# Kernel optimization log

Measured on AMD Instinct MI355X. Metric: run time of the kernel, lower is better.

Reference implementation:

```python
import jax, jax.numpy as jnp
import numpy as np

N_NODES = 150000
N_EDGES = 300000
N_LG_EDGES = 600000
N_TREE = 60000
HIDDEN = 256
DEPTH = 4
ATOM_FDIM = 35
BOND_FDIM = 5
NUM_GRAPHS = 2048


def setup_inputs() -> dict:
    key = jax.random.key(0)
    ks = jax.random.split(key, 14)
    return {
        "node_x": jax.random.normal(ks[0], (N_NODES, ATOM_FDIM), dtype=jnp.float32),
        "bond_x": jax.random.normal(ks[1], (N_EDGES, BOND_FDIM), dtype=jnp.float32),
        "tree_mess": jax.random.normal(ks[2], (N_TREE, HIDDEN), dtype=jnp.float32),
        "W_i": jax.random.normal(ks[3], (ATOM_FDIM + BOND_FDIM, HIDDEN), dtype=jnp.float32) * 0.05,
        "W_h": jax.random.normal(ks[4], (HIDDEN, HIDDEN), dtype=jnp.float32) * 0.05,
        "W_o": jax.random.normal(ks[5], (ATOM_FDIM + HIDDEN, HIDDEN), dtype=jnp.float32) * 0.05,
        "b_o": jax.random.normal(ks[6], (HIDDEN,), dtype=jnp.float32) * 0.05,
        "edge_src": jax.random.randint(ks[7], (N_EDGES,), 0, N_NODES, dtype=jnp.int64 if jax.config.jax_enable_x64 else jnp.int32).astype(jnp.int32),
        "edge_dst": jax.random.randint(ks[8], (N_EDGES,), 0, N_NODES).astype(jnp.int32),
        "lg_src": jax.random.randint(ks[9], (N_LG_EDGES,), 0, N_EDGES).astype(jnp.int32),
        "lg_dst": jax.random.randint(ks[10], (N_LG_EDGES,), 0, N_EDGES).astype(jnp.int32),
        "tgt_nodes": jax.random.randint(ks[11], (N_TREE,), 0, N_NODES).astype(jnp.int32),
        "graph_ids": jnp.sort(jax.random.randint(ks[12], (N_NODES,), 0, NUM_GRAPHS)).astype(jnp.int32),
        "num_graphs": NUM_GRAPHS,
    }


def reference(node_x, bond_x, tree_mess, W_i, W_h, W_o, b_o,
              edge_src, edge_dst, lg_src, lg_dst, tgt_nodes, graph_ids, num_graphs):
    n_nodes = node_x.shape[0]
    n_edges = bond_x.shape[0]

    # msg_input = W_i([src_atom_x ; bond_x])  (no bias)
    features = jnp.concatenate([node_x[edge_src], bond_x], axis=1)  # [E, 40]
    msg_input = features @ W_i                                       # [E, H]
    msg = jax.nn.relu(msg_input)

    # tree-message alpha: scatter_add tree messages onto target atoms (non-PAPER branch)
    node_alpha = jnp.zeros((n_nodes, msg.shape[1]), msg.dtype).at[tgt_nodes].add(tree_mess)
    edge_alpha = node_alpha[edge_src]  # apply_edges: alpha = src['alpha']

    # loopy BP on the line graph: accum = sum of incoming line-graph messages
    def body(msg, _):
        accum = jax.ops.segment_sum(msg[lg_src], lg_dst, num_segments=n_edges)
        msg = jax.nn.relu(msg_input + (accum + edge_alpha) @ W_h)
        return msg, None

    msg, _ = jax.lax.scan(body, msg, None, length=DEPTH - 1)

    # gather: m[v] = sum of msg over incoming edges; h = relu(W_o([x ; m + alpha]) + b)
    m = jax.ops.segment_sum(msg, edge_dst, num_segments=n_nodes)
    h = jax.nn.relu(jnp.concatenate([node_x, m + node_alpha], axis=1) @ W_o + b_o)

    # mean_nodes per graph
    counts = jax.ops.segment_sum(jnp.ones((n_nodes,), h.dtype), graph_ids, num_segments=num_graphs)
    g_sum = jax.ops.segment_sum(h, graph_ids, num_segments=num_graphs)
    g_repr = g_sum / jnp.maximum(counts, 1.0)[:, None]
    return g_repr
```

## Files before the change

### kernel.cpp

```cpp
#include <hip/hip_runtime.h>
#include <stdint.h>

#define HID 256
#define CAP 16

typedef __attribute__((ext_vector_type(8))) short bf16x8;
typedef __attribute__((ext_vector_type(4))) float f32x4;
typedef __attribute__((ext_vector_type(2))) float f32x2;

__device__ __forceinline__ float bf2f(unsigned short u) {
    union { unsigned int i; float f; } v; v.i = ((unsigned int)u) << 16; return v.f;
}
__device__ __forceinline__ unsigned short f2bf(float f) {
    union { float f; unsigned int i; } v; v.f = f;
    unsigned int r = (v.i + 0x7fffu + ((v.i >> 16) & 1u)) >> 16;
    return (unsigned short)r;
}
__device__ __forceinline__ float fp82f_sw(unsigned char b) {
    unsigned int s = (unsigned int)(b & 0x80) << 24;
    int e = (b >> 3) & 0xF;
    int m = b & 7;
    float v;
    if (e) v = __uint_as_float(((unsigned int)(e + 120) << 23) | ((unsigned int)m << 20));
    else   v = (float)m * 0.001953125f;
    return __uint_as_float(__float_as_uint(v) | s);
}
__device__ __forceinline__ unsigned char f2fp8_sw(float x) {
    unsigned int bits = __float_as_uint(x);
    unsigned char s = (unsigned char)((bits >> 24) & 0x80);
    float ax = fabsf(x);
    if (!(ax >= 0.001953125f)) {
        int n = (int)rintf(ax * 512.f);
        return s | (unsigned char)n;
    }
    if (ax >= 448.f) return s | 0x7E;
    int ex; float mant = frexpf(ax, &ex);
    int e = ex + 6;
    if (e >= 1) {
        int q = (int)rintf(mant * 16.f);
        if (q == 16) { q = 8; ++e; }
        if (e > 15 || (e == 15 && q > 14)) return s | 0x7E;
        return s | (unsigned char)((e << 3) | (q - 8));
    } else {
        int n = (int)rintf(ax * 512.f);
        if (n >= 8) return s | 0x08;
        return s | (unsigned char)n;
    }
}
__device__ __forceinline__ unsigned char f2fp8(float x) {
#if __has_builtin(__builtin_amdgcn_cvt_pk_fp8_f32)
    return (unsigned char)(__builtin_amdgcn_cvt_pk_fp8_f32(x, x, 0, false) & 0xff);
#else
    return f2fp8_sw(x);
#endif
}
__device__ __forceinline__ f32x4 fp8x4_to_f32(unsigned int u) {
#if __has_builtin(__builtin_amdgcn_cvt_pk_f32_fp8)
    f32x2 a = __builtin_amdgcn_cvt_pk_f32_fp8(u, false);
    f32x2 b = __builtin_amdgcn_cvt_pk_f32_fp8(u, true);
    f32x4 r; r[0] = a.x; r[1] = a.y; r[2] = b.x; r[3] = b.y;
    return r;
#else
    f32x4 r;
    #pragma unroll
    for (int q = 0; q < 4; ++q) r[q] = fp82f_sw((u >> (8 * q)) & 0xff);
    return r;
#endif
}
__device__ __forceinline__ bf16x8 fp8x8_to_bf16x8(uint2 raw) {
#if __has_builtin(__builtin_amdgcn_cvt_pk_f32_fp8)
    f32x2 p0 = __builtin_amdgcn_cvt_pk_f32_fp8(raw.x, false);
    f32x2 p1 = __builtin_amdgcn_cvt_pk_f32_fp8(raw.x, true);
    f32x2 p2 = __builtin_amdgcn_cvt_pk_f32_fp8(raw.y, false);
    f32x2 p3 = __builtin_amdgcn_cvt_pk_f32_fp8(raw.y, true);
    union { unsigned int u[4]; bf16x8 v; } cv;
    cv.u[0] = (__float_as_uint(p0.x) >> 16) | (__float_as_uint(p0.y) & 0xffff0000u);
    cv.u[1] = (__float_as_uint(p1.x) >> 16) | (__float_as_uint(p1.y) & 0xffff0000u);
    cv.u[2] = (__float_as_uint(p2.x) >> 16) | (__float_as_uint(p2.y) & 0xffff0000u);
    cv.u[3] = (__float_as_uint(p3.x) >> 16) | (__float_as_uint(p3.y) & 0xffff0000u);
    return cv.v;
#else
    union { unsigned short u[8]; bf16x8 v; } cv;
    #pragma unroll
    for (int q = 0; q < 4; ++q) cv.u[q]     = f2bf(fp82f_sw((raw.x >> (8 * q)) & 0xff));
    #pragma unroll
    for (int q = 0; q < 4; ++q) cv.u[4 + q] = f2bf(fp82f_sw((raw.y >> (8 * q)) & 0xff));
    return cv.v;
#endif
}

__device__ __forceinline__ void llds16(const void* g, void* l) {
    __builtin_amdgcn_global_load_lds(
        (const __attribute__((address_space(1))) void*)g,
        (__attribute__((address_space(3))) void*)l, 16, 0, 0);
}


__global__ void k_zero_f(float* __restrict__ p, size_t n) {
    size_t i = (size_t)blockIdx.x * 256 + threadIdx.x;
    if (i < n) p[i] = 0.f;
}
__global__ void k_diag(float* __restrict__ out, float v) {
    if (blockIdx.x == 0 && threadIdx.x == 0) out[0] = v;
}

__global__ void k_init(int* __restrict__ cnt_lg, int E,
                       int* __restrict__ cnt_nd, int* __restrict__ cnt_t, int N,
                       int* __restrict__ gcnt, int* __restrict__ gstart, int G) {
    int i = blockIdx.x * 256 + threadIdx.x;
    if (i < E) cnt_lg[i] = 0;
    if (i < N) { cnt_nd[i] = 0; cnt_t[i] = 0; }
    if (i < G) { gcnt[i] = 0; gstart[i] = N; }
}

__global__ void k_alpha(const float* __restrict__ tm, const int* __restrict__ cnt,
                        const int* __restrict__ bkt, unsigned char* __restrict__ alpha, int N) {
    int wave = threadIdx.x >> 6, lane = threadIdx.x & 63;
    int v = blockIdx.x * 4 + wave;
    if (v >= N) return;
    int d = cnt[v]; if (d > CAP) d = CAP;
    f32x4 s = {0.f, 0.f, 0.f, 0.f};
    const int* bb = bkt + (size_t)v * CAP;
    for (int t = 0; t < d; ++t) {
        int r = bb[t];
        f32x4 x = *(const f32x4*)(tm + (size_t)r * HID + lane * 4);
        #pragma unroll
        for (int k = 0; k < 4; ++k) s[k] += x[k];
    }
    union { unsigned char b[4]; unsigned int u; } ov;
    #pragma unroll
    for (int k = 0; k < 4; ++k) ov.b[k] = f2fp8(s[k]);
    *(unsigned int*)(alpha + (size_t)v * HID + lane * 4) = ov.u;
}

__global__ void k_wt_i(const float* __restrict__ W, unsigned short* __restrict__ Wt) {
    int i = blockIdx.x * 256 + threadIdx.x;
    int n = i >> 6, k = i & 63;
    Wt[i] = f2bf((k < 40) ? W[k * HID + n] : 0.f);
}
__global__ void k_wt_hi(const float* __restrict__ Wh, const float* __restrict__ Wi,
                        unsigned short* __restrict__ Wt) {
    int i = blockIdx.x * 256 + threadIdx.x;
    int n = i / 320, k = i % 320;
    float v;
    if (k < 256) v = Wh[(size_t)k * HID + n];
    else if (k < 296) v = Wi[(size_t)(k - 256) * HID + n];
    else v = 0.f;
    Wt[i] = f2bf(v);
}
__global__ void k_wt_o(const float* __restrict__ W, unsigned short* __restrict__ Wt) {
    int i = blockIdx.x * 256 + threadIdx.x;
    int n = i / 320, k = i % 320;
    float v;
    if (k < 256) v = W[(size_t)(35 + k) * HID + n];
    else if (k < 291) v = W[(size_t)(k - 256) * HID + n];
    else v = 0.f;
    Wt[i] = f2bf(v);
}

__global__ void k_a1(const float* __restrict__ nx, const float* __restrict__ bx,
                     const int* __restrict__ esrc, unsigned char* __restrict__ A1, int E) {
    int i = blockIdx.x * 256 + threadIdx.x;
    if (i >= E * 64) return;
    int e = i >> 6, k = i & 63;
    float v = 0.f;
    if (k < 35) v = nx[(size_t)esrc[e] * 35 + k];
    else if (k < 40) v = bx[(size_t)e * 5 + (k - 35)];
    A1[i] = f2fp8(v);
}

__global__ void k_x1(const float* __restrict__ nx, unsigned char* __restrict__ X1, int N) {
    int i = blockIdx.x * 256 + threadIdx.x;
    if (i >= N * 64) return;
    int v = i >> 6, k = i & 63;
    X1[i] = f2fp8((k < 35) ? nx[(size_t)v * 35 + k] : 0.f);
}

__global__ void k_fill(const int* __restrict__ dst, const int* __restrict__ val,
                       int* __restrict__ cnt, int* __restrict__ bkt, int n, int useval) {
    int i = blockIdx.x * 256 + threadIdx.x;
    if (i >= n) return;
    int d = dst[i];
    int p = atomicAdd(&cnt[d], 1);
    if (p < CAP) bkt[(size_t)d * CAP + p] = useval ? val[i] : i;
}

__global__ void k_gfill(const int* __restrict__ gid, int* __restrict__ gstart,
                        int* __restrict__ gcnt, int N) {
    int i = blockIdx.x * 256 + threadIdx.x;
    if (i >= N) return;
    int g = gid[i];
    atomicAdd(&gcnt[g], 1);
    atomicMin(&gstart[g], i);
}

template<int K1, int KTOT, int EPI, bool PF8, bool QF8, bool OUTF8>
__global__ __launch_bounds__(256, 2)
void gemm4(const void* __restrict__ Ap, int lda1,
           const void* __restrict__ Aq, int lda2,
           const unsigned short* __restrict__ B, int M,
           void* __restrict__ out, const float* __restrict__ bias)
{
    constexpr int NKC = KTOT / 64;
    __shared__ unsigned char Als[128 * 128];
    __shared__ unsigned char Bls[256 * 128];
    const int tid  = threadIdx.x;
    const int lane = tid & 63;
    const int wid  = tid >> 6;
    const int wm = wid & 1, wn = wid >> 1;
    const int row0 = blockIdx.x * 128;
    const int l15  = lane & 15;
    const int quad = lane >> 4;

    f32x4 acc[4][8] = {};

    const int sA8_r = lane >> 2, sA8_c = lane & 3;
    const int s16_r = lane >> 3, s16_c = lane & 7;

    #pragma unroll
    for (int kc = 0; kc < NKC; ++kc) {
        const bool pPart = (kc * 64 < K1);
        const void* As = pPart ? Ap : Aq;
        const int  lda  = pPart ? lda1 : lda2;
        const int  kofs = pPart ? kc * 64 : kc * 64 - K1;
        const bool f8   = pPart ? PF8 : QF8;

        if (f8) {
            #pragma unroll
            for (int t = 0; t < 2; ++t) {
                int r = wid * 32 + t * 16 + sA8_r;
                int ar = row0 + r; if (ar > M - 1) ar = M - 1;
                int ck = sA8_c ^ (r & 3);
                const unsigned char* g = (const unsigned char*)As + (size_t)ar * lda + kofs + ck * 16;
                llds16(g, &Als[(wid * 32 + t * 16) * 64]);
            }
        } else {
            #pragma unroll
            for (int t = 0; t < 4; ++t) {
                int r = wid * 32 + t * 8 + s16_r;
                int ar = row0 + r; if (ar > M - 1) ar = M - 1;
                int ck = s16_c ^ (r & 7);
                const unsigned char* g = (const unsigned char*)As + ((size_t)ar * lda + kofs) * 2 + ck * 16;
                llds16(g, &Als[(wid * 32 + t * 8) * 128]);
            }
        }
        #pragma unroll
        for (int t = 0; t < 8; ++t) {
            int r = wid * 64 + t * 8 + s16_r;
            int ck = s16_c ^ (r & 7);
            const unsigned char* g = (const unsigned char*)B + ((size_t)r * KTOT + kc * 64) * 2 + ck * 16;
            llds16(g, &Bls[(wid * 64 + t * 8) * 128]);
        }
        __syncthreads();

        #pragma unroll
        for (int kk = 0; kk < 64; kk += 32) {
            bf16x8 af[4];
            #pragma unroll
            for (int i = 0; i < 4; ++i) {
                int arow = wm * 64 + i * 16 + l15;
                if (f8) {
                    int ck = (kk >> 4) + (quad >> 1);
                    uint2 raw = *(const uint2*)&Als[arow * 64 + ((ck ^ (arow & 3)) << 4) + ((quad & 1) << 3)];
                    af[i] = fp8x8_to_bf16x8(raw);
                } else {
                    int ck = (kk >> 3) + quad;
                    af[i] = *(const bf16x8*)&Als[arow * 128 + ((ck ^ (arow & 7)) << 4)];
                }
            }
            #pragma unroll
            for (int j = 0; j < 8; ++j) {
                int brow = wn * 128 + j * 16 + l15;
                int ck = (kk >> 3) + quad;
                bf16x8 bfr = *(const bf16x8*)&Bls[brow * 128 + ((ck ^ (brow & 7)) << 4)];
                #pragma unroll
                for (int i = 0; i < 4; ++i)
                    acc[i][j] = __builtin_amdgcn_mfma_f32_16x16x32_bf16(af[i], bfr, acc[i][j], 0, 0, 0);
            }
        }
        if (kc + 1 < NKC) __syncthreads();
    }

    #pragma unroll
    for (int i = 0; i < 4; ++i) {
        int rbase = row0 + wm * 64 + i * 16 + quad * 4;
        #pragma unroll
        for (int r = 0; r < 4; ++r) {
            int row = rbase + r;
            if (row >= M) continue;
            #pragma unroll
            for (int j = 0; j < 8; ++j) {
                int col = wn * 128 + j * 16 + l15;
                float v = acc[i][j][r];
                if (EPI == 1) v += bias[col];
                v = v > 0.f ? v : 0.f;
                if (OUTF8) ((unsigned char*)out)[(size_t)row * HID + col] = f2fp8(v);
                else       ((unsigned short*)out)[(size_t)row * HID + col] = f2bf(v);
            }
        }
    }
}


__global__ void k_accum(const unsigned char* __restrict__ msg, const unsigned char* __restrict__ alpha,
                        const int* __restrict__ esrc, const int* __restrict__ cnt,
                        const int* __restrict__ bkt, unsigned char* __restrict__ accum, int E)
{
    int tid  = threadIdx.x;
    int lane = tid & 63, wave = tid >> 6;
    int sub  = lane >> 4;
    int sl   = lane & 15;
    int e = blockIdx.x * 16 + wave * 4 + sub;
    if (e >= E) return;
    int c = sl * 16;
    int src = esrc[e];
    int d = cnt[e]; if (d > CAP) d = CAP;
    uint4 au = *(const uint4*)(alpha + (size_t)src * HID + c);
    f32x4 s0 = fp8x4_to_f32(au.x);
    f32x4 s1 = fp8x4_to_f32(au.y);
    f32x4 s2 = fp8x4_to_f32(au.z);
    f32x4 s3 = fp8x4_to_f32(au.w);
    const int* bb = bkt + (size_t)e * CAP;
    for (int base = 0; base < d; base += 4) {
        int4 bi = *(const int4*)(bb + base);
        int rem = d - base;
        int i0 = bi.x;
        int i1 = (rem > 1) ? bi.y : bi.x;
        int i2 = (rem > 2) ? bi.z : bi.x;
        int i3 = (rem > 3) ? bi.w : bi.x;
        uint4 m0 = *(const uint4*)(msg + (size_t)i0 * HID + c);
        uint4 m1 = *(const uint4*)(msg + (size_t)i1 * HID + c);
        uint4 m2 = *(const uint4*)(msg + (size_t)i2 * HID + c);
        uint4 m3 = *(const uint4*)(msg + (size_t)i3 * HID + c);
        {   f32x4 a0 = fp8x4_to_f32(m0.x), a1 = fp8x4_to_f32(m0.y), a2 = fp8x4_to_f32(m0.z), a3 = fp8x4_to_f32(m0.w);
            #pragma unroll
            for (int k = 0; k < 4; ++k) { s0[k] += a0[k]; s1[k] += a1[k]; s2[k] += a2[k]; s3[k] += a3[k]; } }
        if (rem > 1) { f32x4 a0 = fp8x4_to_f32(m1.x), a1 = fp8x4_to_f32(m1.y), a2 = fp8x4_to_f32(m1.z), a3 = fp8x4_to_f32(m1.w);
            #pragma unroll
            for (int k = 0; k < 4; ++k) { s0[k] += a0[k]; s1[k] += a1[k]; s2[k] += a2[k]; s3[k] += a3[k]; } }
        if (rem > 2) { f32x4 a0 = fp8x4_to_f32(m2.x), a1 = fp8x4_to_f32(m2.y), a2 = fp8x4_to_f32(m2.z), a3 = fp8x4_to_f32(m2.w);
            #pragma unroll
            for (int k = 0; k < 4; ++k) { s0[k] += a0[k]; s1[k] += a1[k]; s2[k] += a2[k]; s3[k] += a3[k]; } }
        if (rem > 3) { f32x4 a0 = fp8x4_to_f32(m3.x), a1 = fp8x4_to_f32(m3.y), a2 = fp8x4_to_f32(m3.z), a3 = fp8x4_to_f32(m3.w);
            #pragma unroll
            for (int k = 0; k < 4; ++k) { s0[k] += a0[k]; s1[k] += a1[k]; s2[k] += a2[k]; s3[k] += a3[k]; } }
    }
    union { unsigned char b[16]; uint4 u; } ov;
    #pragma unroll
    for (int k = 0; k < 4; ++k) {
        ov.b[k]      = f2fp8(s0[k]);
        ov.b[4 + k]  = f2fp8(s1[k]);
        ov.b[8 + k]  = f2fp8(s2[k]);
        ov.b[12 + k] = f2fp8(s3[k]);
    }
    *(uint4*)(accum + (size_t)e * HID + c) = ov.u;
}

__global__ void k_mpa(const unsigned char* __restrict__ msg, const unsigned char* __restrict__ alpha,
                      const int* __restrict__ cnt, const int* __restrict__ bkt,
                      unsigned short* __restrict__ Mb, int N)
{
    int wave = threadIdx.x >> 6;
    int lane = threadIdx.x & 63;
    int sub  = lane >> 5;
    int sl   = lane & 31;
    int v = blockIdx.x * 8 + wave * 2 + sub;
    if (v >= N) return;
    int c = sl * 8;
    int d = cnt[v]; if (d > CAP) d = CAP;
    uint2 au = *(const uint2*)(alpha + (size_t)v * HID + c);
    f32x4 s0 = fp8x4_to_f32(au.x);
    f32x4 s1 = fp8x4_to_f32(au.y);
    const int* bb = bkt + (size_t)v * CAP;
    for (int base = 0; base < d; base += 4) {
        int4 bi = *(const int4*)(bb + base);
        int rem = d - base;
        int i0 = bi.x;
        int i1 = (rem > 1) ? bi.y : bi.x;
        int i2 = (rem > 2) ? bi.z : bi.x;
        int i3 = (rem > 3) ? bi.w : bi.x;
        uint2 m0 = *(const uint2*)(msg + (size_t)i0 * HID + c);
        uint2 m1 = *(const uint2*)(msg + (size_t)i1 * HID + c);
        uint2 m2 = *(const uint2*)(msg + (size_t)i2 * HID + c);
        uint2 m3 = *(const uint2*)(msg + (size_t)i3 * HID + c);
        {   f32x4 vx = fp8x4_to_f32(m0.x), vy = fp8x4_to_f32(m0.y);
            #pragma unroll
            for (int k = 0; k < 4; ++k) { s0[k] += vx[k]; s1[k] += vy[k]; } }
        if (rem > 1) { f32x4 vx = fp8x4_to_f32(m1.x), vy = fp8x4_to_f32(m1.y);
            #pragma unroll
            for (int k = 0; k < 4; ++k) { s0[k] += vx[k]; s1[k] += vy[k]; } }
        if (rem > 2) { f32x4 vx = fp8x4_to_f32(m2.x), vy = fp8x4_to_f32(m2.y);
            #pragma unroll
            for (int k = 0; k < 4; ++k) { s0[k] += vx[k]; s1[k] += vy[k]; } }
        if (rem > 3) { f32x4 vx = fp8x4_to_f32(m3.x), vy = fp8x4_to_f32(m3.y);
            #pragma unroll
            for (int k = 0; k < 4; ++k) { s0[k] += vx[k]; s1[k] += vy[k]; } }
    }
    union { unsigned short h[8]; uint4 u; } ov;
    #pragma unroll
    for (int k = 0; k < 4; ++k) { ov.h[k] = f2bf(s0[k]); ov.h[4 + k] = f2bf(s1[k]); }
    *(uint4*)(Mb + (size_t)v * HID + c) = ov.u;
}

__global__ void k_gmean(const unsigned short* __restrict__ h, const int* __restrict__ gstart,
                        const int* __restrict__ gcnt, float* __restrict__ out, int G) {
    int g = blockIdx.x;
    int c = threadIdx.x;
    int st = gstart[g], n = gcnt[g];
    float s = 0.f;
    for (int r = 0; r < n; ++r) s += bf2f(h[(size_t)(st + r) * HID + c]);
    out[(size_t)g * HID + c] = (n > 0) ? s / (float)n : 0.f;
}

extern "C" void kernel_launch(void* const* d_in, const int* in_sizes, int n_in,
                              void* d_out, int out_size, void* d_ws, size_t ws_size,
                              hipStream_t stream)
{
    const float* node_x    = (const float*)d_in[0];
    const float* bond_x    = (const float*)d_in[1];
    const float* tree_mess = (const float*)d_in[2];
    const float* W_i       = (const float*)d_in[3];
    const float* W_h       = (const float*)d_in[4];
    const float* W_o       = (const float*)d_in[5];
    const float* b_o       = (const float*)d_in[6];
    const int* edge_src    = (const int*)d_in[7];
    const int* edge_dst    = (const int*)d_in[8];
    const int* lg_src      = (const int*)d_in[9];
    const int* lg_dst      = (const int*)d_in[10];
    const int* tgt_nodes   = (const int*)d_in[11];
    const int* graph_ids   = (const int*)d_in[12];

    const int N = in_sizes[0] / 35;
    const int E = in_sizes[1] / 5;
    const int T = in_sizes[2] / HID;
    const int L = in_sizes[9];
    const int G = out_size / HID;

    auto rup = [](size_t b) { return (b + 255) & ~(size_t)255; };
    const size_t szAcc = (size_t)E * HID;
    const size_t szMsg = (size_t)E * HID;
    const size_t szMbN = (size_t)N * HID * 2;
    const size_t R_acc = rup(szAcc > szMbN ? szAcc : szMbN);
    const size_t R_msg = rup(szMsg > szMbN ? szMsg : szMbN);
    const size_t R_al  = rup((size_t)N * HID);
    const size_t R_a1  = rup((size_t)E * 64);
    const size_t need = R_acc + R_msg + R_al + R_a1
        + rup(256 * 64 * 2) + rup((size_t)256 * 320 * 2) * 2
        + rup((size_t)E * 4) + rup((size_t)E * CAP * 4)
        + rup((size_t)N * 4) + rup((size_t)N * CAP * 4)
        + rup((size_t)N * 4) + rup((size_t)N * CAP * 4)
        + rup((size_t)G * 4) * 2;

    if (need > ws_size) {
        k_zero_f<<<(out_size + 255) / 256, 256, 0, stream>>>((float*)d_out, (size_t)out_size);
        k_diag<<<1, 64, 0, stream>>>((float*)d_out, (float)(ws_size >> 20));
        return;
    }

    char* w = (char*)d_ws;
    auto alloc = [&](size_t bytes) { char* p = w; w += (bytes + 255) & ~(size_t)255; return p; };
    char* r_acc = (char*)alloc(R_acc);
    char* r_msg = (char*)alloc(R_msg);
    char* r_al  = (char*)alloc(R_al);
    char* r_a1  = (char*)alloc(R_a1);
    unsigned short* Wt_i  = (unsigned short*)alloc(256 * 64 * 2);
    unsigned short* Wt_hi = (unsigned short*)alloc((size_t)256 * 320 * 2);
    unsigned short* Wt_o  = (unsigned short*)alloc((size_t)256 * 320 * 2);
    int* cnt_lg = (int*)alloc((size_t)E * 4);
    int* bkt_lg = (int*)alloc((size_t)E * CAP * 4);
    int* cnt_nd = (int*)alloc((size_t)N * 4);
    int* bkt_nd = (int*)alloc((size_t)N * CAP * 4);
    int* cnt_t  = (int*)alloc((size_t)N * 4);
    int* bkt_t  = (int*)alloc((size_t)N * CAP * 4);
    int* gstart = (int*)alloc((size_t)G * 4);
    int* gcnt   = (int*)alloc((size_t)G * 4);

    unsigned char*  accum = (unsigned char*)r_acc;
    unsigned short* Mb    = (unsigned short*)r_acc;
    unsigned char*  msg   = (unsigned char*)r_msg;
    unsigned short* h     = (unsigned short*)r_msg;
    unsigned char*  alpha = (unsigned char*)r_al;
    unsigned char*  A1    = (unsigned char*)r_a1;
    unsigned char*  X1    = (unsigned char*)r_a1;

    k_init<<<(E + 255) / 256, 256, 0, stream>>>(cnt_lg, E, cnt_nd, cnt_t, N, gcnt, gstart, G);

    k_wt_i<<<64, 256, 0, stream>>>(W_i, Wt_i);
    k_wt_hi<<<320, 256, 0, stream>>>(W_h, W_i, Wt_hi);
    k_wt_o<<<320, 256, 0, stream>>>(W_o, Wt_o);
    k_fill<<<(L + 255) / 256, 256, 0, stream>>>(lg_dst, lg_src, cnt_lg, bkt_lg, L, 1);
    k_fill<<<(E + 255) / 256, 256, 0, stream>>>(edge_dst, (const int*)nullptr, cnt_nd, bkt_nd, E, 0);
    k_fill<<<(T + 255) / 256, 256, 0, stream>>>(tgt_nodes, (const int*)nullptr, cnt_t, bkt_t, T, 0);
    k_gfill<<<(N + 255) / 256, 256, 0, stream>>>(graph_ids, gstart, gcnt, N);
    k_alpha<<<(N + 3) / 4, 256, 0, stream>>>(tree_mess, cnt_t, bkt_t, alpha, N);
    k_a1<<<(E * 64 + 255) / 256, 256, 0, stream>>>(node_x, bond_x, edge_src, A1, E);

    dim3 gE((E + 127) / 128, 1), gN((N + 127) / 128, 1);

    gemm4<0, 64, 0, false, true, true><<<gE, 256, 0, stream>>>(nullptr, 0, A1, 64, Wt_i, E, msg, nullptr);

    for (int it = 0; it < 3; ++it) {
        k_accum<<<(E + 15) / 16, 256, 0, stream>>>(msg, alpha, edge_src, cnt_lg, bkt_lg, accum, E);
        gemm4<256, 320, 0, true, true, true><<<gE, 256, 0, stream>>>(accum, 256, A1, 64, Wt_hi, E, msg, nullptr);
    }

    k_x1<<<(N * 64 + 255) / 256, 256, 0, stream>>>(node_x, X1, N);
    k_mpa<<<(N + 7) / 8, 256, 0, stream>>>(msg, alpha, cnt_nd, bkt_nd, Mb, N);
    gemm4<256, 320, 1, false, true, false><<<gN, 256, 0, stream>>>(Mb, 256, X1, 64, Wt_o, N, h, b_o);
    k_gmean<<<G, 256, 0, stream>>>(h, gstart, gcnt, (float*)d_out, G);
}
```

Measured before the change: 856.2 us.

## Fuse setup kernels, vectorize fp8 packing, raise GEMM occupancy, widen gathers

Merges the three weight-transpose kernels into one launch and the four bucket-fill kernels into one. Rewrites the A1 and X1 fp8 packers so each thread emits 16 bytes with one store. Shrinks GEMM shared memory when A is fp8, and raises launch bounds to 4 blocks per CU. Widens the node-gather kernel to 16-byte loads, and unrolls the graph-mean loop into four partial sums. The higher occupancy target can force register spills in the GEMM.

```diff
diff --git a/kernel.cpp b/kernel.cpp
--- a/kernel.cpp
+++ b/kernel.cpp
@@ -113,6 +113,21 @@
     if (i < G) { gcnt[i] = 0; gstart[i] = N; }
 }
 
+__global__ void k_fills(const int* __restrict__ lg_dst, const int* __restrict__ lg_src,
+                        int* __restrict__ cnt_lg, int* __restrict__ bkt_lg, int L,
+                        const int* __restrict__ edst, int* __restrict__ cnt_nd,
+                        int* __restrict__ bkt_nd, int E,
+                        const int* __restrict__ tgt, int* __restrict__ cnt_t,
+                        int* __restrict__ bkt_t, int T,
+                        const int* __restrict__ gid, int* __restrict__ gstart,
+                        int* __restrict__ gcnt, int N) {
+    int i = blockIdx.x * 256 + threadIdx.x;
+    if (i < L) { int d = lg_dst[i]; int p = atomicAdd(&cnt_lg[d], 1); if (p < CAP) bkt_lg[(size_t)d * CAP + p] = lg_src[i]; }
+    if (i < E) { int d = edst[i];   int p = atomicAdd(&cnt_nd[d], 1); if (p < CAP) bkt_nd[(size_t)d * CAP + p] = i; }
+    if (i < T) { int d = tgt[i];    int p = atomicAdd(&cnt_t[d], 1);  if (p < CAP) bkt_t[(size_t)d * CAP + p] = i; }
+    if (i < N) { int g = gid[i]; atomicAdd(&gcnt[g], 1); atomicMin(&gstart[g], i); }
+}
+
 __global__ void k_alpha(const float* __restrict__ tm, const int* __restrict__ cnt,
                         const int* __restrict__ bkt, unsigned char* __restrict__ alpha, int N) {
     int wave = threadIdx.x >> 6, lane = threadIdx.x & 63;
@@ -133,76 +148,74 @@
     *(unsigned int*)(alpha + (size_t)v * HID + lane * 4) = ov.u;
 }
 
-__global__ void k_wt_i(const float* __restrict__ W, unsigned short* __restrict__ Wt) {
+__global__ void k_wt(const float* __restrict__ Wi, const float* __restrict__ Wh,
+                     const float* __restrict__ Wo,
+                     unsigned short* __restrict__ Wt_i, unsigned short* __restrict__ Wt_hi,
+                     unsigned short* __restrict__ Wt_o) {
     int i = blockIdx.x * 256 + threadIdx.x;
-    int n = i >> 6, k = i & 63;
-    Wt[i] = f2bf((k < 40) ? W[k * HID + n] : 0.f);
-}
-__global__ void k_wt_hi(const float* __restrict__ Wh, const float* __restrict__ Wi,
-                        unsigned short* __restrict__ Wt) {
-    int i = blockIdx.x * 256 + threadIdx.x;
-    int n = i / 320, k = i % 320;
-    float v;
-    if (k < 256) v = Wh[(size_t)k * HID + n];
-    else if (k < 296) v = Wi[(size_t)(k - 256) * HID + n];
-    else v = 0.f;
-    Wt[i] = f2bf(v);
-}
-__global__ void k_wt_o(const float* __restrict__ W, unsigned short* __restrict__ Wt) {
-    int i = blockIdx.x * 256 + threadIdx.x;
-    int n = i / 320, k = i % 320;
-    float v;
-    if (k < 256) v = W[(size_t)(35 + k) * HID + n];
-    else if (k < 291) v = W[(size_t)(k - 256) * HID + n];
-    else v = 0.f;
-    Wt[i] = f2bf(v);
+    if (i < 256 * 64) {
+        int n = i >> 6, k = i & 63;
+        Wt_i[i] = f2bf((k < 40) ? Wi[k * HID + n] : 0.f);
+    }
+    if (i < 256 * 320) {
+        int n = i / 320, k = i % 320;
+        float v, u;
+        if (k < 256) v = Wh[(size_t)k * HID + n];
+        else if (k < 296) v = Wi[(size_t)(k - 256) * HID + n];
+        else v = 0.f;
+        Wt_hi[i] = f2bf(v);
+        if (k < 256) u = Wo[(size_t)(35 + k) * HID + n];
+        else if (k < 291) u = Wo[(size_t)(k - 256) * HID + n];
+        else u = 0.f;
+        Wt_o[i] = f2bf(u);
+    }
 }
 
 __global__ void k_a1(const float* __restrict__ nx, const float* __restrict__ bx,
                      const int* __restrict__ esrc, unsigned char* __restrict__ A1, int E) {
     int i = blockIdx.x * 256 + threadIdx.x;
-    if (i >= E * 64) return;
-    int e = i >> 6, k = i & 63;
-    float v = 0.f;
-    if (k < 35) v = nx[(size_t)esrc[e] * 35 + k];
-    else if (k < 40) v = bx[(size_t)e * 5 + (k - 35)];
-    A1[i] = f2fp8(v);
+    int e = i >> 2, q = i & 3;
+    if (e >= E) return;
+    int src = esrc[e];
+    const float* row = nx + (size_t)src * 35;
+    int base = q * 16;
+    union { unsigned char b[16]; uint4 u; } ov;
+    #pragma unroll
+    for (int k = 0; k < 16; ++k) {
+        int col = base + k;
+        float v = 0.f;
+        if (col < 35) v = row[col];
+        else if (col < 40) v = bx[(size_t)e * 5 + (col - 35)];
+        ov.b[k] = f2fp8(v);
+    }
+    *(uint4*)(A1 + (size_t)e * 64 + base) = ov.u;
 }
 
 __global__ void k_x1(const float* __restrict__ nx, unsigned char* __restrict__ X1, int N) {
     int i = blockIdx.x * 256 + threadIdx.x;
-    if (i >= N * 64) return;
-    int v = i >> 6, k = i & 63;
-    X1[i] = f2fp8((k < 35) ? nx[(size_t)v * 35 + k] : 0.f);
-}
-
-__global__ void k_fill(const int* __restrict__ dst, const int* __restrict__ val,
-                       int* __restrict__ cnt, int* __restrict__ bkt, int n, int useval) {
-    int i = blockIdx.x * 256 + threadIdx.x;
-    if (i >= n) return;
-    int d = dst[i];
-    int p = atomicAdd(&cnt[d], 1);
-    if (p < CAP) bkt[(size_t)d * CAP + p] = useval ? val[i] : i;
-}
-
-__global__ void k_gfill(const int* __restrict__ gid, int* __restrict__ gstart,
-                        int* __restrict__ gcnt, int N) {
-    int i = blockIdx.x * 256 + threadIdx.x;
-    if (i >= N) return;
-    int g = gid[i];
-    atomicAdd(&gcnt[g], 1);
-    atomicMin(&gstart[g], i);
+    int v = i >> 2, q = i & 3;
+    if (v >= N) return;
+    const float* row = nx + (size_t)v * 35;
+    int base = q * 16;
+    union { unsigned char b[16]; uint4 u; } ov;
+    #pragma unroll
+    for (int k = 0; k < 16; ++k) {
+        int col = base + k;
+        ov.b[k] = f2fp8((col < 35) ? row[col] : 0.f);
+    }
+    *(uint4*)(X1 + (size_t)v * 64 + base) = ov.u;
 }
 
 template<int K1, int KTOT, int EPI, bool PF8, bool QF8, bool OUTF8>
-__global__ __launch_bounds__(256, 2)
+__global__ __launch_bounds__(256, 4)
 void gemm4(const void* __restrict__ Ap, int lda1,
            const void* __restrict__ Aq, int lda2,
            const unsigned short* __restrict__ B, int M,
            void* __restrict__ out, const float* __restrict__ bias)
 {
     constexpr int NKC = KTOT / 64;
-    __shared__ unsigned char Als[128 * 128];
+    constexpr bool ABF = (K1 > 0 && !PF8) || (KTOT > K1 && !QF8);
+    __shared__ unsigned char Als[ABF ? 128 * 128 : 128 * 64];
     __shared__ unsigned char Bls[256 * 128];
     const int tid  = threadIdx.x;
     const int lane = tid & 63;
@@ -360,17 +373,19 @@
                       const int* __restrict__ cnt, const int* __restrict__ bkt,
                       unsigned short* __restrict__ Mb, int N)
 {
-    int wave = threadIdx.x >> 6;
-    int lane = threadIdx.x & 63;
-    int sub  = lane >> 5;
-    int sl   = lane & 31;
-    int v = blockIdx.x * 8 + wave * 2 + sub;
+    int tid  = threadIdx.x;
+    int lane = tid & 63, wave = tid >> 6;
+    int sub  = lane >> 4;
+    int sl   = lane & 15;
+    int v = blockIdx.x * 16 + wave * 4 + sub;
     if (v >= N) return;
-    int c = sl * 8;
+    int c = sl * 16;
     int d = cnt[v]; if (d > CAP) d = CAP;
-    uint2 au = *(const uint2*)(alpha + (size_t)v * HID + c);
+    uint4 au = *(const uint4*)(alpha + (size_t)v * HID + c);
     f32x4 s0 = fp8x4_to_f32(au.x);
     f32x4 s1 = fp8x4_to_f32(au.y);
+    f32x4 s2 = fp8x4_to_f32(au.z);
+    f32x4 s3 = fp8x4_to_f32(au.w);
     const int* bb = bkt + (size_t)v * CAP;
     for (int base = 0; base < d; base += 4) {
         int4 bi = *(const int4*)(bb + base);
@@ -379,27 +394,31 @@
         int i1 = (rem > 1) ? bi.y : bi.x;
         int i2 = (rem > 2) ? bi.z : bi.x;
         int i3 = (rem > 3) ? bi.w : bi.x;
-        uint2 m0 = *(const uint2*)(msg + (size_t)i0 * HID + c);
-        uint2 m1 = *(const uint2*)(msg + (size_t)i1 * HID + c);
-        uint2 m2 = *(const uint2*)(msg + (size_t)i2 * HID + c);
-        uint2 m3 = *(const uint2*)(msg + (size_t)i3 * HID + c);
-        {   f32x4 vx = fp8x4_to_f32(m0.x), vy = fp8x4_to_f32(m0.y);
-            #pragma unroll
-            for (int k = 0; k < 4; ++k) { s0[k] += vx[k]; s1[k] += vy[k]; } }
-        if (rem > 1) { f32x4 vx = fp8x4_to_f32(m1.x), vy = fp8x4_to_f32(m1.y);
-            #pragma unroll
-            for (int k = 0; k < 4; ++k) { s0[k] += vx[k]; s1[k] += vy[k]; } }
-        if (rem > 2) { f32x4 vx = fp8x4_to_f32(m2.x), vy = fp8x4_to_f32(m2.y);
-            #pragma unroll
-            for (int k = 0; k < 4; ++k) { s0[k] += vx[k]; s1[k] += vy[k]; } }
-        if (rem > 3) { f32x4 vx = fp8x4_to_f32(m3.x), vy = fp8x4_to_f32(m3.y);
-            #pragma unroll
-            for (int k = 0; k < 4; ++k) { s0[k] += vx[k]; s1[k] += vy[k]; } }
-    }
-    union { unsigned short h[8]; uint4 u; } ov;
-    #pragma unroll
-    for (int k = 0; k < 4; ++k) { ov.h[k] = f2bf(s0[k]); ov.h[4 + k] = f2bf(s1[k]); }
-    *(uint4*)(Mb + (size_t)v * HID + c) = ov.u;
+        uint4 m0 = *(const uint4*)(msg + (size_t)i0 * HID + c);
+        uint4 m1 = *(const uint4*)(msg + (size_t)i1 * HID + c);
+        uint4 m2 = *(const uint4*)(msg + (size_t)i2 * HID + c);
+        uint4 m3 = *(const uint4*)(msg + (size_t)i3 * HID + c);
+        {   f32x4 a0 = fp8x4_to_f32(m0.x), a1 = fp8x4_to_f32(m0.y), a2 = fp8x4_to_f32(m0.z), a3 = fp8x4_to_f32(m0.w);
+            #pragma unroll
+            for (int k = 0; k < 4; ++k) { s0[k] += a0[k]; s1[k] += a1[k]; s2[k] += a2[k]; s3[k] += a3[k]; } }
+        if (rem > 1) { f32x4 a0 = fp8x4_to_f32(m1.x), a1 = fp8x4_to_f32(m1.y), a2 = fp8x4_to_f32(m1.z), a3 = fp8x4_to_f32(m1.w);
+            #pragma unroll
+            for (int k = 0; k < 4; ++k) { s0[k] += a0[k]; s1[k] += a1[k]; s2[k] += a2[k]; s3[k] += a3[k]; } }
+        if (rem > 2) { f32x4 a0 = fp8x4_to_f32(m2.x), a1 = fp8x4_to_f32(m2.y), a2 = fp8x4_to_f32(m2.z), a3 = fp8x4_to_f32(m2.w);
+            #pragma unroll
+            for (int k = 0; k < 4; ++k) { s0[k] += a0[k]; s1[k] += a1[k]; s2[k] += a2[k]; s3[k] += a3[k]; } }
+        if (rem > 3) { f32x4 a0 = fp8x4_to_f32(m3.x), a1 = fp8x4_to_f32(m3.y), a2 = fp8x4_to_f32(m3.z), a3 = fp8x4_to_f32(m3.w);
+            #pragma unroll
+            for (int k = 0; k < 4; ++k) { s0[k] += a0[k]; s1[k] += a1[k]; s2[k] += a2[k]; s3[k] += a3[k]; } }
+    }
+    union { unsigned short h[8]; uint4 u; } o1, o2;
+    #pragma unroll
+    for (int k = 0; k < 4; ++k) {
+        o1.h[k] = f2bf(s0[k]); o1.h[4 + k] = f2bf(s1[k]);
+        o2.h[k] = f2bf(s2[k]); o2.h[4 + k] = f2bf(s3[k]);
+    }
+    *(uint4*)(Mb + (size_t)v * HID + c)     = o1.u;
+    *(uint4*)(Mb + (size_t)v * HID + c + 8) = o2.u;
 }
 
 __global__ void k_gmean(const unsigned short* __restrict__ h, const int* __restrict__ gstart,
@@ -407,8 +426,16 @@
     int g = blockIdx.x;
     int c = threadIdx.x;
     int st = gstart[g], n = gcnt[g];
-    float s = 0.f;
-    for (int r = 0; r < n; ++r) s += bf2f(h[(size_t)(st + r) * HID + c]);
+    float s0 = 0.f, s1 = 0.f, s2 = 0.f, s3 = 0.f;
+    int r = 0;
+    for (; r + 4 <= n; r += 4) {
+        s0 += bf2f(h[(size_t)(st + r) * HID + c]);
+        s1 += bf2f(h[(size_t)(st + r + 1) * HID + c]);
+        s2 += bf2f(h[(size_t)(st + r + 2) * HID + c]);
+        s3 += bf2f(h[(size_t)(st + r + 3) * HID + c]);
+    }
+    float s = (s0 + s1) + (s2 + s3);
+    for (; r < n; ++r) s += bf2f(h[(size_t)(st + r) * HID + c]);
     out[(size_t)g * HID + c] = (n > 0) ? s / (float)n : 0.f;
 }
 
@@ -484,16 +511,13 @@
     unsigned char*  X1    = (unsigned char*)r_a1;
 
     k_init<<<(E + 255) / 256, 256, 0, stream>>>(cnt_lg, E, cnt_nd, cnt_t, N, gcnt, gstart, G);
-
-    k_wt_i<<<64, 256, 0, stream>>>(W_i, Wt_i);
-    k_wt_hi<<<320, 256, 0, stream>>>(W_h, W_i, Wt_hi);
-    k_wt_o<<<320, 256, 0, stream>>>(W_o, Wt_o);
-    k_fill<<<(L + 255) / 256, 256, 0, stream>>>(lg_dst, lg_src, cnt_lg, bkt_lg, L, 1);
-    k_fill<<<(E + 255) / 256, 256, 0, stream>>>(edge_dst, (const int*)nullptr, cnt_nd, bkt_nd, E, 0);
-    k_fill<<<(T + 255) / 256, 256, 0, stream>>>(tgt_nodes, (const int*)nullptr, cnt_t, bkt_t, T, 0);
-    k_gfill<<<(N + 255) / 256, 256, 0, stream>>>(graph_ids, gstart, gcnt, N);
+    k_wt<<<320, 256, 0, stream>>>(W_i, W_h, W_o, Wt_i, Wt_hi, Wt_o);
+    k_fills<<<(L + 255) / 256, 256, 0, stream>>>(lg_dst, lg_src, cnt_lg, bkt_lg, L,
+                                                 edge_dst, cnt_nd, bkt_nd, E,
+                                                 tgt_nodes, cnt_t, bkt_t, T,
+                                                 graph_ids, gstart, gcnt, N);
     k_alpha<<<(N + 3) / 4, 256, 0, stream>>>(tree_mess, cnt_t, bkt_t, alpha, N);
-    k_a1<<<(E * 64 + 255) / 256, 256, 0, stream>>>(node_x, bond_x, edge_src, A1, E);
+    k_a1<<<(E * 4 + 255) / 256, 256, 0, stream>>>(node_x, bond_x, edge_src, A1, E);
 
     dim3 gE((E + 127) / 128, 1), gN((N + 127) / 128, 1);
 
@@ -504,8 +528,8 @@
         gemm4<256, 320, 0, true, true, true><<<gE, 256, 0, stream>>>(accum, 256, A1, 64, Wt_hi, E, msg, nullptr);
     }
 
-    k_x1<<<(N * 64 + 255) / 256, 256, 0, stream>>>(node_x, X1, N);
-    k_mpa<<<(N + 7) / 8, 256, 0, stream>>>(msg, alpha, cnt_nd, bkt_nd, Mb, N);
+    k_x1<<<(N * 4 + 255) / 256, 256, 0, stream>>>(node_x, X1, N);
+    k_mpa<<<(N + 15) / 16, 256, 0, stream>>>(msg, alpha, cnt_nd, bkt_nd, Mb, N);
     gemm4<256, 320, 1, false, true, false><<<gN, 256, 0, stream>>>(Mb, 256, X1, 64, Wt_o, N, h, b_o);
     k_gmean<<<G, 256, 0, stream>>>(h, gstart, gcnt, (float*)d_out, G);
 }
```

Result: slower. 1.865 ms (+117.9%).
